# Kernel tuning notes

Hardware: AMD Instinct MI355X
Metric: run time of the kernel (lower is better)

The kernel has to match this reference:

```python
import jax, jax.numpy as jnp
import numpy as np

VOL = (32, 64, 64)          # 3D brain volume grid
B, N, D = 2, 4096, 1024     # batch, active voxels (seq_len), feature_dim
H, KNN = 16, 16             # num_heads, num_neighbors


def setup_inputs() -> dict:
    key = jax.random.key(0)
    k1, k2, k3, k4 = jax.random.split(key, 4)
    # boolean 3D mask with exactly N active voxels (so seq_len == #active)
    rng = np.random.default_rng(0)
    flat = np.zeros(int(np.prod(VOL)), dtype=bool)
    flat[rng.choice(flat.size, N, replace=False)] = True
    visual_cortex_mask = jnp.asarray(flat.reshape(VOL))
    x = jax.random.normal(k1, (B, N, D), dtype=jnp.float32)
    s = 1.0 / np.sqrt(D)
    Wq = jax.random.normal(k2, (D, D), dtype=jnp.float32) * s
    Wk = jax.random.normal(k3, (D, D), dtype=jnp.float32) * s
    Wv = jax.random.normal(k4, (D, D), dtype=jnp.float32) * s
    return {"x": x, "visual_cortex_mask": visual_cortex_mask,
            "Wq": Wq, "Wk": Wk, "Wv": Wv}


def reference(x, visual_cortex_mask, Wq, Wk, Wv):
    batch, seq_len, d = x.shape
    hd = d // H
    # --- kNN over active voxel coordinates (cdist + topk) ---
    flat = visual_cortex_mask.reshape(-1)
    (act,) = jnp.nonzero(flat, size=seq_len)  # flat indices of active voxels
    coords = jnp.stack(jnp.unravel_index(act, visual_cortex_mask.shape),
                       axis=1).astype(jnp.float32)           # [N, 3]
    sq = jnp.sum(coords * coords, axis=-1)                    # [N]
    d2 = sq[:, None] + sq[None, :] - 2.0 * (coords @ coords.T)  # squared dists
    _, nbr = jax.lax.top_k(-d2, KNN + 1)   # smallest distances first
    nbr = nbr[:, 1:]                       # drop self -> [N, KNN] positions
    # --- QKV projections (torch Linear: x @ W.T) ---
    q = (x @ Wq.T).reshape(batch, seq_len, H, hd)
    k = (x @ Wk.T).reshape(batch, seq_len, H, hd)
    v = (x @ Wv.T).reshape(batch, seq_len, H, hd)
    # --- gather-based sparse attention: each query attends only to its
    # KNN neighbors (exactly the block-mask semantics of the original) ---
    kn = k[:, nbr]   # [B, N, KNN, H, hd]
    vn = v[:, nbr]   # [B, N, KNN, H, hd]
    scale = 1.0 / np.sqrt(hd)
    scores = jnp.einsum('bnhd,bnkhd->bhnk', q, kn) * scale
    attn = jax.nn.softmax(scores, axis=-1)
    out = jnp.einsum('bhnk,bnkhd->bnhd', attn, vn).reshape(batch, seq_len, d)
    metric = k.mean(axis=2)  # key.mean over heads -> [B, N, hd]
    return out, metric
```

## Files before the change

### kernel.cpp

```cpp
#include <hip/hip_runtime.h>
#include <hip/hip_bf16.h>
#include <stdint.h>

#define BATCH 2
#define NPTS 4096
#define DMODEL 1024
#define NHEAD 16
#define HDIM 64
#define KNN 16
#define MASKN 131072
#define EBLK 128

typedef __attribute__((ext_vector_type(8))) short bf16x8;
typedef __attribute__((ext_vector_type(4))) float f32x4;

__device__ __forceinline__ float b2f(unsigned short u) {
    union { unsigned int i; float f; } c; c.i = ((unsigned int)u) << 16; return c.f;
}
__device__ __forceinline__ unsigned short f2b(float f) {
    unsigned int x = __float_as_uint(f);
    unsigned int r = (x + 0x7fffu + ((x >> 16) & 1u)) >> 16;
    return (unsigned short)r;
}
__device__ __forceinline__ unsigned int pack2f(float a, float b) {
    return (unsigned int)f2b(a) | ((unsigned int)f2b(b) << 16);
}
__device__ __forceinline__ void gload16(const unsigned short* g, unsigned short* l) {
    __builtin_amdgcn_global_load_lds((const __attribute__((address_space(1))) void*)g,
                                     (__attribute__((address_space(3))) void*)l, 16, 0, 0);
}

__global__ __launch_bounds__(256) void count8_kernel(const unsigned char* __restrict__ m8,
                                                     int* __restrict__ cnt8) {
    __shared__ int red[256];
    const int b = blockIdx.x, t = threadIdx.x;
    const uchar4 v = ((const uchar4*)m8)[b * 256 + t];
    red[t] = (v.x != 0) + (v.y != 0) + (v.z != 0) + (v.w != 0);
    __syncthreads();
    for (int off = 128; off >= 1; off >>= 1) {
        if (t < off) red[t] += red[t + off];
        __syncthreads();
    }
    if (t == 0) cnt8[b] = red[0];
}

__global__ __launch_bounds__(256) void count32_kernel(const unsigned char* __restrict__ m8,
                                                      const int* __restrict__ cnt8,
                                                      int* __restrict__ cnt32) {
    __shared__ int red[256];
    const int b = blockIdx.x, t = threadIdx.x;
    red[t] = (t < EBLK) ? cnt8[t] : 0;
    __syncthreads();
    for (int off = 128; off >= 1; off >>= 1) {
        if (t < off) red[t] += red[t + off];
        __syncthreads();
    }
    if (red[0] == NPTS) return;
    __syncthreads();
    const int4 v = ((const int4*)m8)[b * 256 + t];
    red[t] = (v.x != 0) + (v.y != 0) + (v.z != 0) + (v.w != 0);
    __syncthreads();
    for (int off = 128; off >= 1; off >>= 1) {
        if (t < off) red[t] += red[t + off];
        __syncthreads();
    }
    if (t == 0) cnt32[b] = red[0];
}

__global__ __launch_bounds__(256) void extract_kernel(const unsigned char* __restrict__ m8,
                                                      const int* __restrict__ cnt8,
                                                      const int* __restrict__ cnt32,
                                                      int* __restrict__ act) {
    __shared__ int sblk[EBLK];
    __shared__ int sthr[256];
    const int b = blockIdx.x, t = threadIdx.x;
    if (t < EBLK) sblk[t] = cnt8[t];
    __syncthreads();
    for (int off = 1; off < EBLK; off <<= 1) {
        int v = (t < EBLK && t >= off) ? sblk[t - off] : 0;
        __syncthreads();
        if (t < EBLK) sblk[t] += v;
        __syncthreads();
    }
    const bool bytes = (sblk[EBLK - 1] == NPTS);
    if (!bytes) {
        __syncthreads();
        if (t < EBLK) sblk[t] = cnt32[t];
        __syncthreads();
        for (int off = 1; off < EBLK; off <<= 1) {
            int v = (t < EBLK && t >= off) ? sblk[t - off] : 0;
            __syncthreads();
            if (t < EBLK) sblk[t] += v;
            __syncthreads();
        }
    }
    const int blkoff = (b == 0) ? 0 : sblk[b - 1];
    const int gbase = b * 1024 + t * 4;
    int f0, f1, f2, f3;
    if (bytes) {
        const uchar4 v = ((const uchar4*)m8)[b * 256 + t];
        f0 = v.x != 0; f1 = v.y != 0; f2 = v.z != 0; f3 = v.w != 0;
    } else {
        const int4 v = ((const int4*)m8)[b * 256 + t];
        f0 = v.x != 0; f1 = v.y != 0; f2 = v.z != 0; f3 = v.w != 0;
    }
    const int c = f0 + f1 + f2 + f3;
    sthr[t] = c;
    __syncthreads();
    for (int off = 1; off < 256; off <<= 1) {
        int v = (t >= off) ? sthr[t - off] : 0;
        __syncthreads();
        sthr[t] += v;
        __syncthreads();
    }
    int pos = blkoff + sthr[t] - c;
    if (f0) act[pos++] = gbase;
    if (f1) act[pos++] = gbase + 1;
    if (f2) act[pos++] = gbase + 2;
    if (f3) act[pos++] = gbase + 3;
}

__global__ __launch_bounds__(256) void knn_kernel(const int* __restrict__ act,
                                                  int* __restrict__ nbr) {
    __shared__ int act_s[NPTS];
    const int t = threadIdx.x;
    for (int i = t; i < NPTS; i += 256) act_s[i] = act[i];
    __syncthreads();
    const int q = blockIdx.x * 16 + (t >> 4);
    const int sub = t & 15;
    const int aq = act_s[q];
    const int qz = aq >> 12, qy = (aq >> 6) & 63, qx = aq & 63;
    int best[17];
    #pragma unroll
    for (int i = 0; i < 17; ++i) best[i] = 0x7FFFFFFF;
    for (int j = sub; j < NPTS; j += 16) {
        const int aj = act_s[j];
        const int dz = (aj >> 12) - qz;
        const int dy = ((aj >> 6) & 63) - qy;
        const int dx = (aj & 63) - qx;
        const int d2 = dz * dz + dy * dy + dx * dx;
        int p = (d2 << 12) | j;
        if (p < best[16]) {
            #pragma unroll
            for (int u = 0; u < 17; ++u) {
                const bool lt = p < best[u];
                const int tmp = best[u];
                best[u] = lt ? p : best[u];
                p = lt ? tmp : p;
            }
        }
    }
    int head = best[0];
    int keep = 0;
    #pragma unroll
    for (int r = 0; r < KNN + 1; ++r) {
        int m = head;
        #pragma unroll
        for (int off = 8; off >= 1; off >>= 1) m = min(m, __shfl_xor(m, off, 16));
        if (sub == r - 1) keep = m;
        const bool win = (head == m);
        #pragma unroll
        for (int u = 0; u < 16; ++u) if (win) best[u] = best[u + 1];
        if (win) best[16] = 0x7FFFFFFF;
        head = best[0];
    }
    nbr[q * KNN + sub] = keep & 4095;
}

__global__ __launch_bounds__(256) void cast_kernel(const float* __restrict__ src,
                                                   unsigned short* __restrict__ dst, int n8) {
    const int i = blockIdx.x * 256 + threadIdx.x;
    if (i >= n8) return;
    const float4 a = ((const float4*)src)[2 * i];
    const float4 b = ((const float4*)src)[2 * i + 1];
    uint4 w;
    w.x = pack2f(a.x, a.y); w.y = pack2f(a.z, a.w);
    w.z = pack2f(b.x, b.y); w.w = pack2f(b.z, b.w);
    ((uint4*)dst)[i] = w;
}

__global__ __launch_bounds__(256) void gemm_qkv_bf16(
    const unsigned short* __restrict__ Xb,
    const unsigned short* __restrict__ Wb,
    unsigned short* __restrict__ O0, unsigned short* __restrict__ O1, unsigned short* __restrict__ O2)
{
    const int K = DMODEL, N = DMODEL;
    const unsigned short* W = Wb + (size_t)blockIdx.z * DMODEL * DMODEL;
    unsigned short* C = (blockIdx.z == 0) ? O0 : (blockIdx.z == 1) ? O1 : O2;
    __shared__ unsigned short As[2][128 * 32];
    __shared__ unsigned short Bs[2][128 * 32];
    const int tid = threadIdx.x;
    const int rowBase = blockIdx.x * 128;
    const int colBase = blockIdx.y * 128;
    const int lane = tid & 63, w = tid >> 6;
    const int wr = w >> 1, wc = w & 1;
    const int lr = lane & 15, kg = lane >> 4;

    f32x4 acc[4][4];
    const f32x4 zero = {0.f, 0.f, 0.f, 0.f};
    #pragma unroll
    for (int i = 0; i < 4; ++i)
        #pragma unroll
        for (int j = 0; j < 4; ++j) acc[i][j] = zero;

    const int srow4 = tid >> 2;
    const int xch = (tid & 3) ^ (srow4 & 3);
    const unsigned short* agp = &Xb[(size_t)(rowBase + srow4) * K + xch * 8];
    const unsigned short* bgp = &W[(size_t)(colBase + srow4) * K + xch * 8];
    unsigned short* a0[2] = { &As[0][w * 512], &As[1][w * 512] };
    unsigned short* a1[2] = { &As[0][2048 + w * 512], &As[1][2048 + w * 512] };
    unsigned short* b0[2] = { &Bs[0][w * 512], &Bs[1][w * 512] };
    unsigned short* b1[2] = { &Bs[0][2048 + w * 512], &Bs[1][2048 + w * 512] };

    #define STAGE(kt, bf) do { \
        gload16(agp + (kt) * 32,           a0[bf]); \
        gload16(agp + 64 * K + (kt) * 32,  a1[bf]); \
        gload16(bgp + (kt) * 32,           b0[bf]); \
        gload16(bgp + 64 * K + (kt) * 32,  b1[bf]); \
    } while (0)

    const int rchunk = (kg ^ (lr & 3)) * 8;

    #define COMPUTE(bf) do { \
        bf16x8 af[4], bfr[4]; \
        _Pragma("unroll") \
        for (int mi = 0; mi < 4; ++mi) \
            af[mi] = *(const bf16x8*)&As[bf][(wr * 64 + mi * 16 + lr) * 32 + rchunk]; \
        _Pragma("unroll") \
        for (int ni = 0; ni < 4; ++ni) \
            bfr[ni] = *(const bf16x8*)&Bs[bf][(wc * 64 + ni * 16 + lr) * 32 + rchunk]; \
        __builtin_amdgcn_s_setprio(1); \
        _Pragma("unroll") \
        for (int mi = 0; mi < 4; ++mi) \
            _Pragma("unroll") \
            for (int ni = 0; ni < 4; ++ni) \
                acc[mi][ni] = __builtin_amdgcn_mfma_f32_16x16x32_bf16(af[mi], bfr[ni], acc[mi][ni], 0, 0, 0); \
        __builtin_amdgcn_s_setprio(0); \
    } while (0)

    STAGE(0, 0);
    STAGE(1, 1);
    for (int kt = 0; kt < 30; ++kt) {
        const int bf = kt & 1;
        asm volatile("s_waitcnt vmcnt(4)" ::: "memory");
        __builtin_amdgcn_s_barrier();
        COMPUTE(bf);
        __builtin_amdgcn_s_barrier();
        STAGE(kt + 2, bf);
    }
    asm volatile("s_waitcnt vmcnt(4)" ::: "memory");
    __builtin_amdgcn_s_barrier();
    COMPUTE(0);
    __builtin_amdgcn_s_barrier();
    asm volatile("s_waitcnt vmcnt(0)" ::: "memory");
    __builtin_amdgcn_s_barrier();
    COMPUTE(1);
    #undef STAGE
    #undef COMPUTE

    #pragma unroll
    for (int mi = 0; mi < 4; ++mi)
        #pragma unroll
        for (int ni = 0; ni < 4; ++ni) {
            const int row0 = rowBase + wr * 64 + mi * 16 + kg * 4;
            const int col = colBase + wc * 64 + ni * 16 + lr;
            #pragma unroll
            for (int j = 0; j < 4; ++j)
                C[(size_t)(row0 + j) * N + col] = f2b(acc[mi][ni][j]);
        }
}

__device__ __forceinline__ void stage16(unsigned short* dst, const float* src) {
    const float4 a = ((const float4*)src)[0];
    const float4 b = ((const float4*)src)[1];
    const float4 c = ((const float4*)src)[2];
    const float4 d = ((const float4*)src)[3];
    uint4 w0, w1;
    w0.x = pack2f(a.x, a.y); w0.y = pack2f(a.z, a.w);
    w0.z = pack2f(b.x, b.y); w0.w = pack2f(b.z, b.w);
    w1.x = pack2f(c.x, c.y); w1.y = pack2f(c.z, c.w);
    w1.z = pack2f(d.x, d.y); w1.w = pack2f(d.z, d.w);
    ((uint4*)dst)[0] = w0;
    ((uint4*)dst)[1] = w1;
}

__global__ __launch_bounds__(256) void gemm_qkv_f32(
    const float* __restrict__ X,
    const float* __restrict__ W0, const float* __restrict__ W1, const float* __restrict__ W2,
    unsigned short* __restrict__ O0, unsigned short* __restrict__ O1, unsigned short* __restrict__ O2)
{
    const int K = DMODEL, N = DMODEL;
    const float* W = (blockIdx.z == 0) ? W0 : (blockIdx.z == 1) ? W1 : W2;
    unsigned short* C = (blockIdx.z == 0) ? O0 : (blockIdx.z == 1) ? O1 : O2;
    __shared__ unsigned short As[128 * 32];
    __shared__ unsigned short Bs[128 * 32];
    const int tid = threadIdx.x;
    const int rowBase = blockIdx.x * 128;
    const int colBase = blockIdx.y * 128;
    const int lane = tid & 63, w = tid >> 6;
    const int wr = w >> 1, wc = w & 1;
    const int lr = lane & 15, kg = lane >> 4;
    const int srow = tid >> 1;
    const int scol = (tid & 1) * 16;
    f32x4 acc[4][4];
    const f32x4 zero = {0.f, 0.f, 0.f, 0.f};
    #pragma unroll
    for (int i = 0; i < 4; ++i)
        #pragma unroll
        for (int j = 0; j < 4; ++j) acc[i][j] = zero;
    const float* Arow = &X[(size_t)(rowBase + srow) * K + scol];
    const float* Brow = &W[(size_t)(colBase + srow) * K + scol];
    unsigned short* Adst = &As[srow * 32 + scol];
    unsigned short* Bdst = &Bs[srow * 32 + scol];
    for (int kb = 0; kb < K; kb += 32) {
        __syncthreads();
        stage16(Adst, Arow + kb);
        stage16(Bdst, Brow + kb);
        __syncthreads();
        bf16x8 af[4], bfr[4];
        #pragma unroll
        for (int mi = 0; mi < 4; ++mi)
            af[mi] = *(const bf16x8*)&As[(wr * 64 + mi * 16 + lr) * 32 + kg * 8];
        #pragma unroll
        for (int ni = 0; ni < 4; ++ni)
            bfr[ni] = *(const bf16x8*)&Bs[(wc * 64 + ni * 16 + lr) * 32 + kg * 8];
        #pragma unroll
        for (int mi = 0; mi < 4; ++mi)
            #pragma unroll
            for (int ni = 0; ni < 4; ++ni)
                acc[mi][ni] = __builtin_amdgcn_mfma_f32_16x16x32_bf16(af[mi], bfr[ni], acc[mi][ni], 0, 0, 0);
    }
    #pragma unroll
    for (int mi = 0; mi < 4; ++mi)
        #pragma unroll
        for (int ni = 0; ni < 4; ++ni) {
            const int row0 = rowBase + wr * 64 + mi * 16 + kg * 4;
            const int col = colBase + wc * 64 + ni * 16 + lr;
            #pragma unroll
            for (int j = 0; j < 4; ++j)
                C[(size_t)(row0 + j) * N + col] = f2b(acc[mi][ni][j]);
        }
}

__global__ __launch_bounds__(256) void attn_kernel(
    const unsigned short* __restrict__ Q, const unsigned short* __restrict__ Kb,
    const unsigned short* __restrict__ Vb, const int* __restrict__ nbr,
    float* __restrict__ out)
{
    const int n = blockIdx.x;
    const int b = blockIdx.y;
    __shared__ unsigned short k_s[128][KNN][8];
    __shared__ unsigned short q_s[DMODEL];
    __shared__ float a_s[NHEAD][KNN];
    __shared__ int nb_s[KNN];
    const int tid = threadIdx.x;
    if (tid < KNN) nb_s[tid] = nbr[n * KNN + tid];
    *(int2*)&q_s[tid * 4] = *(const int2*)&Q[((size_t)b * NPTS + n) * DMODEL + tid * 4];
    __syncthreads();
    {
        const int kk = tid & 15;
        const int c0 = tid >> 4;
        const unsigned short* krow = &Kb[((size_t)b * NPTS + nb_s[kk]) * DMODEL];
        #pragma unroll
        for (int i = 0; i < 8; ++i) {
            const int c = c0 + 16 * i;
            *(uint4*)&k_s[c][kk][0] = *(const uint4*)&krow[c * 8];
        }
    }
    const int o = tid * 4;
    ushort4 vpre[KNN];
    #pragma unroll
    for (int k2 = 0; k2 < KNN; ++k2)
        vpre[k2] = *(const ushort4*)&Vb[((size_t)b * NPTS + nb_s[k2]) * DMODEL + o];
    __syncthreads();
    const int h = tid >> 4, kk = tid & 15;
    float s = 0.f;
    #pragma unroll
    for (int j = 0; j < 8; ++j) {
        const bf16x8 qq = *(const bf16x8*)&q_s[h * HDIM + j * 8];
        const bf16x8 kr = *(const bf16x8*)&k_s[h * 8 + j][kk][0];
        #pragma unroll
        for (int e = 0; e < 8; ++e)
            s += b2f((unsigned short)qq[e]) * b2f((unsigned short)kr[e]);
    }
    s *= 0.125f;
    float m = s;
    #pragma unroll
    for (int off = 8; off >= 1; off >>= 1) m = fmaxf(m, __shfl_xor(m, off, 16));
    const float e = __expf(s - m);
    float sum = e;
    #pragma unroll
    for (int off = 8; off >= 1; off >>= 1) sum += __shfl_xor(sum, off, 16);
    a_s[h][kk] = e / sum;
    __syncthreads();
    const int h2 = tid >> 4;
    float av0 = 0.f, av1 = 0.f, av2 = 0.f, av3 = 0.f;
    #pragma unroll
    for (int k2 = 0; k2 < KNN; ++k2) {
        const float a = a_s[h2][k2];
        av0 += a * b2f(vpre[k2].x); av1 += a * b2f(vpre[k2].y);
        av2 += a * b2f(vpre[k2].z); av3 += a * b2f(vpre[k2].w);
    }
    float4 r; r.x = av0; r.y = av1; r.z = av2; r.w = av3;
    *(float4*)&out[((size_t)b * NPTS + n) * DMODEL + o] = r;
}

__global__ __launch_bounds__(256) void metric_kernel(const unsigned short* __restrict__ Kb,
                                                     float* __restrict__ mout) {
    const int i = blockIdx.x * 256 + threadIdx.x;
    if (i >= BATCH * NPTS * HDIM) return;
    const int d = i & 63;
    const int bn = i >> 6;
    const unsigned short* kp = &Kb[(size_t)bn * DMODEL + d];
    float s = 0.f;
    #pragma unroll
    for (int hh = 0; hh < NHEAD; ++hh) s += b2f(kp[hh * HDIM]);
    mout[i] = s * 0.0625f;
}

extern "C" void kernel_launch(void* const* d_in, const int* in_sizes, int n_in,
                              void* d_out, int out_size, void* d_ws, size_t ws_size,
                              hipStream_t stream) {
    const float* x = (const float*)d_in[0];
    const unsigned char* mask = (const unsigned char*)d_in[1];
    const float* Wq = (const float*)d_in[2];
    const float* Wk = (const float*)d_in[3];
    const float* Wv = (const float*)d_in[4];
    float* out = (float*)d_out;
    char* ws = (char*)d_ws;

    const size_t QKV_BYTES = (size_t)BATCH * NPTS * DMODEL * 2;
    const size_t XB_BYTES  = (size_t)BATCH * NPTS * DMODEL * 2;
    const size_t WB_BYTES  = (size_t)3 * DMODEL * DMODEL * 2;
    unsigned short* qb = (unsigned short*)(ws);
    unsigned short* kb = (unsigned short*)(ws + QKV_BYTES);
    unsigned short* vb = (unsigned short*)(ws + 2 * QKV_BYTES);
    const size_t SMALL_BYTES = (size_t)NPTS * sizeof(int) * (1 + KNN) + 2 * EBLK * sizeof(int);
    const size_t need_base = 3 * QKV_BYTES + SMALL_BYTES;
    const size_t need_full = need_base + XB_BYTES + WB_BYTES;
    const bool full = (ws_size >= need_full);
    char* tail = ws + 3 * QKV_BYTES;
    unsigned short* Xb = (unsigned short*)tail;
    unsigned short* Wb = (unsigned short*)(tail + XB_BYTES);
    char* small = full ? (tail + XB_BYTES + WB_BYTES) : tail;
    int* act  = (int*)small;
    int* nbr  = (int*)(small + NPTS * sizeof(int));
    int* cnt8 = (int*)(small + NPTS * sizeof(int) * (1 + KNN));
    int* cnt32 = cnt8 + EBLK;
    if (ws_size < need_base) return;

    count8_kernel<<<EBLK, 256, 0, stream>>>(mask, cnt8);
    count32_kernel<<<EBLK, 256, 0, stream>>>(mask, cnt8, cnt32);
    extract_kernel<<<EBLK, 256, 0, stream>>>(mask, cnt8, cnt32, act);
    knn_kernel<<<256, 256, 0, stream>>>(act, nbr);
    if (full) {
        const int xn8 = BATCH * NPTS * DMODEL / 8;
        const int wn8 = DMODEL * DMODEL / 8;
        cast_kernel<<<(xn8 + 255) / 256, 256, 0, stream>>>(x, Xb, xn8);
        cast_kernel<<<(wn8 + 255) / 256, 256, 0, stream>>>(Wq, Wb, wn8);
        cast_kernel<<<(wn8 + 255) / 256, 256, 0, stream>>>(Wk, Wb + (size_t)DMODEL * DMODEL, wn8);
        cast_kernel<<<(wn8 + 255) / 256, 256, 0, stream>>>(Wv, Wb + (size_t)2 * DMODEL * DMODEL, wn8);
        gemm_qkv_bf16<<<dim3(64, 8, 3), 256, 0, stream>>>(Xb, Wb, qb, kb, vb);
    } else {
        gemm_qkv_f32<<<dim3(64, 8, 3), 256, 0, stream>>>(x, Wq, Wk, Wv, qb, kb, vb);
    }
    attn_kernel<<<dim3(NPTS, BATCH), 256, 0, stream>>>(qb, kb, vb, nbr, out);
    metric_kernel<<<(BATCH * NPTS * HDIM + 255) / 256, 256, 0, stream>>>(kb, out + (size_t)BATCH * NPTS * DMODEL);
}
```

Before: 202.4 us.

## Widen kNN to wave-per-query, merge cast launches, XCD-aware GEMM block mapping

The kNN kernel now gives each query a full 64-lane wavefront instead of 16 lanes and launches four times as many blocks, so the per-lane candidate scan is shorter and more CUs stay busy. The four separate fp32-to-bf16 cast launches are merged into one kernel that picks its source and destination by index, which removes launch overhead. The QKV GEMM grid is flattened to 1D and remapped so that consecutive row tiles land on the same XCD, which is meant to improve L2 reuse of the shared X and W tiles. The wider kNN reduction uses more shuffle steps per round, and the grid remap assumes a round-robin XCD dispatch order.

```diff
diff --git a/kernel.cpp b/kernel.cpp
--- a/kernel.cpp
+++ b/kernel.cpp
@@ -126,14 +126,14 @@
     const int t = threadIdx.x;
     for (int i = t; i < NPTS; i += 256) act_s[i] = act[i];
     __syncthreads();
-    const int q = blockIdx.x * 16 + (t >> 4);
-    const int sub = t & 15;
+    const int q = blockIdx.x * 4 + (t >> 6);
+    const int lane = t & 63;
     const int aq = act_s[q];
     const int qz = aq >> 12, qy = (aq >> 6) & 63, qx = aq & 63;
     int best[17];
     #pragma unroll
     for (int i = 0; i < 17; ++i) best[i] = 0x7FFFFFFF;
-    for (int j = sub; j < NPTS; j += 16) {
+    for (int j = lane; j < NPTS; j += 64) {
         const int aj = act_s[j];
         const int dz = (aj >> 12) - qz;
         const int dy = ((aj >> 6) & 63) - qy;
@@ -156,27 +156,44 @@
     for (int r = 0; r < KNN + 1; ++r) {
         int m = head;
         #pragma unroll
-        for (int off = 8; off >= 1; off >>= 1) m = min(m, __shfl_xor(m, off, 16));
-        if (sub == r - 1) keep = m;
+        for (int off = 32; off >= 1; off >>= 1) m = min(m, __shfl_xor(m, off, 64));
+        if (lane == r - 1) keep = m;
         const bool win = (head == m);
         #pragma unroll
         for (int u = 0; u < 16; ++u) if (win) best[u] = best[u + 1];
         if (win) best[16] = 0x7FFFFFFF;
         head = best[0];
     }
-    nbr[q * KNN + sub] = keep & 4095;
-}
-
-__global__ __launch_bounds__(256) void cast_kernel(const float* __restrict__ src,
-                                                   unsigned short* __restrict__ dst, int n8) {
+    if (lane < KNN) nbr[q * KNN + lane] = keep & 4095;
+}
+
+#define XN8 (BATCH * NPTS * DMODEL / 8)
+#define WN8 (DMODEL * DMODEL / 8)
+__global__ __launch_bounds__(256) void cast_all_kernel(
+    const float* __restrict__ x, const float* __restrict__ wq,
+    const float* __restrict__ wk, const float* __restrict__ wv,
+    unsigned short* __restrict__ Xb, unsigned short* __restrict__ Wb) {
     const int i = blockIdx.x * 256 + threadIdx.x;
-    if (i >= n8) return;
-    const float4 a = ((const float4*)src)[2 * i];
-    const float4 b = ((const float4*)src)[2 * i + 1];
+    const int total = XN8 + 3 * WN8;
+    if (i >= total) return;
+    const float* src;
+    unsigned short* dst;
+    if (i < XN8) {
+        src = x + (size_t)i * 8;
+        dst = Xb + (size_t)i * 8;
+    } else {
+        const int j = i - XN8;
+        const int wsel = j >> 17;
+        const int o = j & (WN8 - 1);
+        src = ((wsel == 0) ? wq : (wsel == 1) ? wk : wv) + (size_t)o * 8;
+        dst = Wb + ((size_t)wsel * WN8 + o) * 8;
+    }
+    const float4 a = ((const float4*)src)[0];
+    const float4 b = ((const float4*)src)[1];
     uint4 w;
     w.x = pack2f(a.x, a.y); w.y = pack2f(a.z, a.w);
     w.z = pack2f(b.x, b.y); w.w = pack2f(b.z, b.w);
-    ((uint4*)dst)[i] = w;
+    *(uint4*)dst = w;
 }
 
 __global__ __launch_bounds__(256) void gemm_qkv_bf16(
@@ -185,13 +202,20 @@
     unsigned short* __restrict__ O0, unsigned short* __restrict__ O1, unsigned short* __restrict__ O2)
 {
     const int K = DMODEL, N = DMODEL;
-    const unsigned short* W = Wb + (size_t)blockIdx.z * DMODEL * DMODEL;
-    unsigned short* C = (blockIdx.z == 0) ? O0 : (blockIdx.z == 1) ? O1 : O2;
+    const int bid = blockIdx.x;
+    const int xcd = bid & 7;
+    const int idx = bid >> 3;
+    const int x   = xcd * 8 + (idx & 7);
+    const int yz  = idx >> 3;
+    const int y   = yz & 7;
+    const int z   = yz >> 3;
+    const unsigned short* W = Wb + (size_t)z * DMODEL * DMODEL;
+    unsigned short* C = (z == 0) ? O0 : (z == 1) ? O1 : O2;
     __shared__ unsigned short As[2][128 * 32];
     __shared__ unsigned short Bs[2][128 * 32];
     const int tid = threadIdx.x;
-    const int rowBase = blockIdx.x * 128;
-    const int colBase = blockIdx.y * 128;
+    const int rowBase = x * 128;
+    const int colBase = y * 128;
     const int lane = tid & 63, w = tid >> 6;
     const int wr = w >> 1, wc = w & 1;
     const int lr = lane & 15, kg = lane >> 4;
@@ -452,15 +476,11 @@
     count8_kernel<<<EBLK, 256, 0, stream>>>(mask, cnt8);
     count32_kernel<<<EBLK, 256, 0, stream>>>(mask, cnt8, cnt32);
     extract_kernel<<<EBLK, 256, 0, stream>>>(mask, cnt8, cnt32, act);
-    knn_kernel<<<256, 256, 0, stream>>>(act, nbr);
+    knn_kernel<<<1024, 256, 0, stream>>>(act, nbr);
     if (full) {
-        const int xn8 = BATCH * NPTS * DMODEL / 8;
-        const int wn8 = DMODEL * DMODEL / 8;
-        cast_kernel<<<(xn8 + 255) / 256, 256, 0, stream>>>(x, Xb, xn8);
-        cast_kernel<<<(wn8 + 255) / 256, 256, 0, stream>>>(Wq, Wb, wn8);
-        cast_kernel<<<(wn8 + 255) / 256, 256, 0, stream>>>(Wk, Wb + (size_t)DMODEL * DMODEL, wn8);
-        cast_kernel<<<(wn8 + 255) / 256, 256, 0, stream>>>(Wv, Wb + (size_t)2 * DMODEL * DMODEL, wn8);
-        gemm_qkv_bf16<<<dim3(64, 8, 3), 256, 0, stream>>>(Xb, Wb, qb, kb, vb);
+        const int castN = XN8 + 3 * WN8;
+        cast_all_kernel<<<(castN + 255) / 256, 256, 0, stream>>>(x, Wq, Wk, Wv, Xb, Wb);
+        gemm_qkv_bf16<<<dim3(1536), 256, 0, stream>>>(Xb, Wb, qb, kb, vb);
     } else {
         gemm_qkv_f32<<<dim3(64, 8, 3), 256, 0, stream>>>(x, Wq, Wk, Wv, qb, kb, vb);
     }
```

After: 183.8 us. 1.1x faster.
